# Kernel tuning notes

Hardware: AMD Instinct MI355X
Metric: run time of the kernel (lower is better)

Reference implementation:

```python
import jax, jax.numpy as jnp
import numpy as np

DILATION = 512
C_RES = 128
C_SKIP = 256


def setup_inputs() -> dict:
    key = jax.random.key(0)
    ks = jax.random.split(key, 6)
    B, T = 8, 16384
    x = jax.random.normal(ks[0], (B, C_RES, T), dtype=jnp.float32)
    # dilated conv weight: [out_ch, in_ch, kernel=2], no bias
    w_dil = jax.random.normal(ks[1], (C_RES, C_RES, 2), dtype=jnp.float32) * (1.0 / np.sqrt(2 * C_RES))
    # 1x1 residual conv (with bias)
    w_res = jax.random.normal(ks[2], (C_RES, C_RES), dtype=jnp.float32) * (1.0 / np.sqrt(C_RES))
    b_res = jax.random.normal(ks[3], (C_RES,), dtype=jnp.float32) * 0.01
    # 1x1 skip conv (with bias)
    w_skip = jax.random.normal(ks[4], (C_SKIP, C_RES), dtype=jnp.float32) * (1.0 / np.sqrt(C_RES))
    b_skip = jax.random.normal(ks[5], (C_SKIP,), dtype=jnp.float32) * 0.01
    return {"x": x, "w_dil": w_dil, "w_res": w_res, "b_res": b_res,
            "w_skip": w_skip, "b_skip": b_skip, "skip_size": 4096}


def reference(x, w_dil, w_res, b_res, w_skip, b_skip, skip_size):
    # x: [B, C, T]. Dilated causal conv, kernel_size=2, dilation=DILATION, no padding:
    # pre[:, :, t] = W[:,:,0] @ x[:,:,t] + W[:,:,1] @ x[:,:,t+DILATION], t in [0, T-DILATION)
    T = x.shape[2]
    L = T - DILATION  # output length
    pre = (jnp.einsum('oi,bit->bot', w_dil[:, :, 0], x[:, :, :L]) +
           jnp.einsum('oi,bit->bot', w_dil[:, :, 1], x[:, :, DILATION:]))
    activated = jnp.tanh(pre) * jax.nn.sigmoid(pre)  # filter * gate
    # 1x1 residual conv + residual add with the time-aligned tail of x
    out = (jnp.einsum('oi,bit->bot', w_res, activated) + b_res[None, :, None]
           + x[:, :, T - L:])
    # 1x1 skip conv, keep last skip_size steps
    skip = jnp.einsum('oi,bit->bot', w_skip, activated) + b_skip[None, :, None]
    skip = skip[:, :, -skip_size:]
    return (out, skip)
```

## Files before the change

kernel.cpp:

```cpp
#include <hip/hip_runtime.h>

typedef float f32x4 __attribute__((ext_vector_type(4)));
typedef __bf16 bf16x8 __attribute__((ext_vector_type(8)));

__device__ __forceinline__ unsigned short f2bf(float f) {
  unsigned u = __builtin_bit_cast(unsigned, f);
  u = (u + 0x7FFFu + ((u >> 16) & 1u)) >> 16;
  return (unsigned short)u;
}

__device__ __forceinline__ f32x4 MFMA16(uint4 a, uint4 b, f32x4 c) {
  return __builtin_amdgcn_mfma_f32_16x16x32_bf16(
      __builtin_bit_cast(bf16x8, a), __builtin_bit_cast(bf16x8, b), c, 0, 0, 0);
}

__global__ void wn_prep(const float* __restrict__ wd, const float* __restrict__ wres,
                        const float* __restrict__ wskip, unsigned short* __restrict__ ws16) {
  int g = blockIdx.x * 256 + threadIdx.x;
  if (g < 32768) {
    int kc = g >> 12, rem = g & 4095;
    int o = rem >> 5, kl = rem & 31;
    int k = kc * 32 + kl;
    int tap = k >> 7, i = k & 127;
    ws16[g] = f2bf(wd[(o << 8) + (i << 1) + tap]);
  } else {
    int g2 = g - 32768;
    int pkk = g2 >> 12;
    int rem = g2 & 4095;
    int o = rem >> 5, kl = rem & 31;
    int p = pkk >> 2, kk = pkk & 3;
    int k = kk * 32 + kl;
    float v = (p == 0) ? wres[o * 128 + k] : wskip[((p - 1) * 128 + o) * 128 + k];
    ws16[32768 + g2] = f2bf(v);
  }
}

__global__ __launch_bounds__(256, 4) void wn_main(
    const float* __restrict__ x,
    const float* __restrict__ bres_g,
    const float* __restrict__ bskip_g,
    const unsigned short* __restrict__ wd2_img,
    const unsigned short* __restrict__ wrs2_img,
    float* __restrict__ out,
    float* __restrict__ skipo) {
  extern __shared__ unsigned short lds[];
  unsigned short* xall = lds;
  unsigned short* actT = lds;

  const int w = blockIdx.x;
  const int b = w & 7;
  const int tile = 247 - (w >> 3);
  const int t0 = tile * 64;

  const int tid = threadIdx.x;
  const int lane = tid & 63;
  const int wv = tid >> 6;
  const int mw = wv >> 1;
  const int nw = wv & 1;
  const int l15 = lane & 15;
  const int lhi = lane >> 4;

  const int kq = tid & 7;
  const int tpr = tid >> 3;

  const float* xb_base = x + (size_t)b * (128 * 16384);

  float2 xr[4][4];

  auto issueX = [&](int kc, int s) {
    int kglob = kc * 32 + kq * 4;
    int tap = kglob >> 7;
    int ib = kglob & 127;
    const float* p = xb_base + (size_t)ib * 16384 + (t0 + tap * 512 + tpr * 2);
    xr[s][0] = *(const float2*)(p);
    xr[s][1] = *(const float2*)(p + 16384);
    xr[s][2] = *(const float2*)(p + 32768);
    xr[s][3] = *(const float2*)(p + 49152);
  };
  auto writeX = [&](int kc, int s) {
    unsigned short* dst = xall + kc * 2304;
    int r0 = tpr * 2;
    ushort4 a0, a1;
    a0.x = f2bf(xr[s][0].x); a0.y = f2bf(xr[s][1].x); a0.z = f2bf(xr[s][2].x); a0.w = f2bf(xr[s][3].x);
    a1.x = f2bf(xr[s][0].y); a1.y = f2bf(xr[s][1].y); a1.z = f2bf(xr[s][2].y); a1.w = f2bf(xr[s][3].y);
    *(ushort4*)(dst + r0 * 36 + kq * 4) = a0;
    *(ushort4*)(dst + (r0 + 1) * 36 + kq * 4) = a1;
  };

  f32x4 acc[4][2];
#pragma unroll
  for (int i = 0; i < 4; ++i)
#pragma unroll
    for (int j = 0; j < 2; ++j) acc[i][j] = (f32x4){0.f, 0.f, 0.f, 0.f};

#pragma unroll
  for (int half = 0; half < 2; ++half) {
#pragma unroll
    for (int c = 0; c < 4; ++c) issueX(half * 4 + c, c);
#pragma unroll
    for (int c = 0; c < 4; ++c) writeX(half * 4 + c, c);
  }
  __syncthreads();

#pragma unroll 2
  for (int kc = 0; kc < 8; ++kc) {
    uint4 af[4];
    const unsigned short* wbase = wd2_img + (kc << 12) + lhi * 8;
#pragma unroll
    for (int mi = 0; mi < 4; ++mi)
      af[mi] = *(const uint4*)(wbase + (mw * 64 + mi * 16 + l15) * 32);
    uint4 bfr[2];
    const unsigned short* xbuf = xall + kc * 2304;
#pragma unroll
    for (int ni = 0; ni < 2; ++ni)
      bfr[ni] = *(const uint4*)(xbuf + (nw * 32 + ni * 16 + l15) * 36 + lhi * 8);
#pragma unroll
    for (int mi = 0; mi < 4; ++mi)
#pragma unroll
      for (int ni = 0; ni < 2; ++ni)
        acc[mi][ni] = MFMA16(af[mi], bfr[ni], acc[mi][ni]);
  }
  __syncthreads();

#pragma unroll
  for (int mi = 0; mi < 4; ++mi) {
#pragma unroll
    for (int ni = 0; ni < 2; ++ni) {
      ushort4 av;
#pragma unroll
      for (int r = 0; r < 4; ++r) {
        float p = acc[mi][ni][r];
        p = fminf(fmaxf(p, -15.f), 15.f);
        float ep = __expf(p);
        float e2 = ep * ep;
        float sg = ep * __builtin_amdgcn_rcpf(1.f + ep);
        float th = (e2 - 1.f) * __builtin_amdgcn_rcpf(e2 + 1.f);
        ((unsigned short*)&av)[r] = f2bf(th * sg);
      }
      int trow = nw * 32 + ni * 16 + l15;
      int o0 = mw * 64 + mi * 16 + lhi * 4;
      *(ushort4*)(actT + trow * 140 + o0) = av;
    }
  }
  __syncthreads();

  const int npass = (tile >= 184) ? 3 : 1;
#pragma unroll 1
  for (int p = 0; p < npass; ++p) {
    f32x4 acc2[4][2];
#pragma unroll
    for (int i = 0; i < 4; ++i)
#pragma unroll
      for (int j = 0; j < 2; ++j) acc2[i][j] = (f32x4){0.f, 0.f, 0.f, 0.f};

#pragma unroll 2
    for (int kk = 0; kk < 4; ++kk) {
      uint4 af[4], bfr[2];
      const unsigned short* wbase = wrs2_img + ((p * 4 + kk) << 12) + lhi * 8;
#pragma unroll
      for (int mi = 0; mi < 4; ++mi)
        af[mi] = *(const uint4*)(wbase + (mw * 64 + mi * 16 + l15) * 32);
#pragma unroll
      for (int ni = 0; ni < 2; ++ni)
        bfr[ni] = *(const uint4*)(actT + (nw * 32 + ni * 16 + l15) * 140 + kk * 32 + lhi * 8);
#pragma unroll
      for (int mi = 0; mi < 4; ++mi)
#pragma unroll
        for (int ni = 0; ni < 2; ++ni)
          acc2[mi][ni] = MFMA16(af[mi], bfr[ni], acc2[mi][ni]);
    }

    if (p == 0) {
#pragma unroll
      for (int mi = 0; mi < 4; ++mi) {
        int o0 = mw * 64 + mi * 16 + lhi * 4;
        float br[4];
#pragma unroll
        for (int r = 0; r < 4; ++r) br[r] = bres_g[o0 + r];
#pragma unroll
        for (int ni = 0; ni < 2; ++ni) {
          int tl = nw * 32 + ni * 16 + l15;
#pragma unroll
          for (int r = 0; r < 4; ++r) {
            size_t row = (size_t)(b * 128 + o0 + r);
            float v = acc2[mi][ni][r] + br[r] + x[row * 16384 + 512 + t0 + tl];
            out[row * 15872 + t0 + tl] = v;
          }
        }
      }
    } else {
#pragma unroll
      for (int mi = 0; mi < 4; ++mi) {
        int o2 = (p - 1) * 128 + mw * 64 + mi * 16 + lhi * 4;
        float bs[4];
#pragma unroll
        for (int r = 0; r < 4; ++r) bs[r] = bskip_g[o2 + r];
#pragma unroll
        for (int ni = 0; ni < 2; ++ni) {
          int tl = nw * 32 + ni * 16 + l15;
          int s = t0 + tl - 11776;
#pragma unroll
          for (int r = 0; r < 4; ++r) {
            skipo[(size_t)(b * 256 + o2 + r) * 4096 + s] = acc2[mi][ni][r] + bs[r];
          }
        }
      }
    }
  }
}

extern "C" void kernel_launch(void* const* d_in, const int* in_sizes, int n_in,
                              void* d_out, int out_size, void* d_ws, size_t ws_size,
                              hipStream_t stream) {
  const float* x      = (const float*)d_in[0];
  const float* w_dil  = (const float*)d_in[1];
  const float* w_res  = (const float*)d_in[2];
  const float* b_res  = (const float*)d_in[3];
  const float* w_skip = (const float*)d_in[4];
  const float* b_skip = (const float*)d_in[5];
  unsigned short* ws16 = (unsigned short*)d_ws;
  float* out = (float*)d_out;
  float* skipo = out + 16252928;

  wn_prep<<<320, 256, 0, stream>>>(w_dil, w_res, w_skip, ws16);

  wn_main<<<1984, 256, 36864, stream>>>(x, b_res, b_skip, ws16, ws16 + 32768, out, skipo);
}
```

Before: 91.65 us.

## Halve LDS x staging buffer with two-phase load to raise occupancy

Stages the input x tile in two halves through a buffer half the previous size, issuing the second half's global loads before computing the first half. This cuts dynamic LDS per block and raises the launch-bounds occupancy target from 4 to 5 blocks. The LDS row stride also changes from 36 to 38 to alter bank mapping. The cost is an extra barrier and write phase mid-kernel, and tighter register limits that could cause spills.

```diff
diff --git a/kernel.cpp b/kernel.cpp
--- a/kernel.cpp
+++ b/kernel.cpp
@@ -35,7 +35,7 @@
   }
 }
 
-__global__ __launch_bounds__(256, 4) void wn_main(
+__global__ __launch_bounds__(256, 5) void wn_main(
     const float* __restrict__ x,
     const float* __restrict__ bres_g,
     const float* __restrict__ bskip_g,
@@ -44,8 +44,8 @@
     float* __restrict__ out,
     float* __restrict__ skipo) {
   extern __shared__ unsigned short lds[];
-  unsigned short* xall = lds;
-  unsigned short* actT = lds;
+  unsigned short* xhalf = lds;
+  unsigned short* actT  = lds;
 
   const int w = blockIdx.x;
   const int b = w & 7;
@@ -78,13 +78,13 @@
     xr[s][3] = *(const float2*)(p + 49152);
   };
   auto writeX = [&](int kc, int s) {
-    unsigned short* dst = xall + kc * 2304;
+    unsigned short* dst = xhalf + (kc & 3) * 2432;
     int r0 = tpr * 2;
     ushort4 a0, a1;
     a0.x = f2bf(xr[s][0].x); a0.y = f2bf(xr[s][1].x); a0.z = f2bf(xr[s][2].x); a0.w = f2bf(xr[s][3].x);
     a1.x = f2bf(xr[s][0].y); a1.y = f2bf(xr[s][1].y); a1.z = f2bf(xr[s][2].y); a1.w = f2bf(xr[s][3].y);
-    *(ushort4*)(dst + r0 * 36 + kq * 4) = a0;
-    *(ushort4*)(dst + (r0 + 1) * 36 + kq * 4) = a1;
+    *(ushort4*)(dst + r0 * 38 + kq * 4) = a0;
+    *(ushort4*)(dst + (r0 + 1) * 38 + kq * 4) = a1;
   };
 
   f32x4 acc[4][2];
@@ -94,26 +94,50 @@
     for (int j = 0; j < 2; ++j) acc[i][j] = (f32x4){0.f, 0.f, 0.f, 0.f};
 
 #pragma unroll
-  for (int half = 0; half < 2; ++half) {
-#pragma unroll
-    for (int c = 0; c < 4; ++c) issueX(half * 4 + c, c);
-#pragma unroll
-    for (int c = 0; c < 4; ++c) writeX(half * 4 + c, c);
-  }
-  __syncthreads();
+  for (int c = 0; c < 4; ++c) issueX(c, c);
+#pragma unroll
+  for (int c = 0; c < 4; ++c) writeX(c, c);
+#pragma unroll
+  for (int c = 0; c < 4; ++c) issueX(4 + c, c);
+  asm volatile("s_waitcnt lgkmcnt(0)" ::: "memory");
+  __builtin_amdgcn_s_barrier();
 
 #pragma unroll 2
-  for (int kc = 0; kc < 8; ++kc) {
+  for (int kc = 0; kc < 4; ++kc) {
     uint4 af[4];
     const unsigned short* wbase = wd2_img + (kc << 12) + lhi * 8;
 #pragma unroll
     for (int mi = 0; mi < 4; ++mi)
       af[mi] = *(const uint4*)(wbase + (mw * 64 + mi * 16 + l15) * 32);
     uint4 bfr[2];
-    const unsigned short* xbuf = xall + kc * 2304;
+    const unsigned short* xbuf = xhalf + kc * 2432;
 #pragma unroll
     for (int ni = 0; ni < 2; ++ni)
-      bfr[ni] = *(const uint4*)(xbuf + (nw * 32 + ni * 16 + l15) * 36 + lhi * 8);
+      bfr[ni] = *(const uint4*)(xbuf + (nw * 32 + ni * 16 + l15) * 38 + lhi * 8);
+#pragma unroll
+    for (int mi = 0; mi < 4; ++mi)
+#pragma unroll
+      for (int ni = 0; ni < 2; ++ni)
+        acc[mi][ni] = MFMA16(af[mi], bfr[ni], acc[mi][ni]);
+  }
+  __syncthreads();
+
+#pragma unroll
+  for (int c = 0; c < 4; ++c) writeX(4 + c, c);
+  __syncthreads();
+
+#pragma unroll 2
+  for (int kc = 4; kc < 8; ++kc) {
+    uint4 af[4];
+    const unsigned short* wbase = wd2_img + (kc << 12) + lhi * 8;
+#pragma unroll
+    for (int mi = 0; mi < 4; ++mi)
+      af[mi] = *(const uint4*)(wbase + (mw * 64 + mi * 16 + l15) * 32);
+    uint4 bfr[2];
+    const unsigned short* xbuf = xhalf + (kc & 3) * 2432;
+#pragma unroll
+    for (int ni = 0; ni < 2; ++ni)
+      bfr[ni] = *(const uint4*)(xbuf + (nw * 32 + ni * 16 + l15) * 38 + lhi * 8);
 #pragma unroll
     for (int mi = 0; mi < 4; ++mi)
 #pragma unroll
@@ -224,5 +248,5 @@
 
   wn_prep<<<320, 256, 0, stream>>>(w_dil, w_res, w_skip, ws16);
 
-  wn_main<<<1984, 256, 36864, stream>>>(x, b_res, b_skip, ws16, ws16 + 32768, out, skipo);
-}
+  wn_main<<<1984, 256, 19456, stream>>>(x, b_res, b_skip, ws16, ws16 + 32768, out, skipo);
+}
```

Result: slower. 105.6 us (+15.2%).
